# Kernel tuning notes

Measured on AMD Instinct MI355X. Metric: run time of the kernel, lower is better.

## Reference

```python
import jax, jax.numpy as jnp
import numpy as np
from jax import lax

THD = 0.8  # Lowe ratio-test threshold (module init kwarg `thd`)


def setup_inputs() -> dict:
    key = jax.random.key(0)
    k1, k2 = jax.random.split(key)
    desc1 = jax.random.normal(k1, (16384, 128), dtype=jnp.float32)
    desc2 = jax.random.normal(k2, (16384, 128), dtype=jnp.float32)
    return {"desc1": desc1, "desc2": desc2}


def _cdist(a, b):
    # Euclidean pairwise distances, (B1, B2), same math as torch.cdist(p=2)
    sq_a = jnp.sum(a * a, axis=-1, keepdims=True)          # (B1, 1)
    sq_b = jnp.sum(b * b, axis=-1)                          # (B2,)
    d2 = sq_a + sq_b - 2.0 * (a @ b.T)                      # (B1, B2)
    return jnp.sqrt(jnp.maximum(d2, 0.0))


def reference(desc1, desc2):
    cost = _cdist(desc1, desc2)                             # (B1, B2)
    # two smallest distances per row
    neg_vals, idxs_in_2 = lax.top_k(-cost, 2)               # (B1, 2) each
    vals = -neg_vals
    ratio = vals[:, 0] / vals[:, 1]                         # (B1,)
    mask = ratio <= THD                                     # (B1,) bool
    # jit-compatible padded outputs: masked-out rows carry 0 distance; the
    # boolean mask selects the valid (idxs_in1, idxs_in2) match rows, which is
    # the compaction torch does with boolean indexing.
    match_dists = jnp.where(mask, ratio, 0.0)               # (B1,)
    idxs_in1 = jnp.arange(desc1.shape[0], dtype=jnp.int32)
    matches_idxs = jnp.stack([idxs_in1, idxs_in_2[:, 0].astype(jnp.int32)], axis=1)  # (B1, 2)
    return match_dists, matches_idxs, mask
```

## Files before the change

kernel.cpp:

```cpp
#include <hip/hip_runtime.h>
#include <math.h>
#include <float.h>
#include <stdint.h>


typedef __attribute__((ext_vector_type(4))) float     f32x4;
typedef __attribute__((ext_vector_type(8))) _Float16  half8;

#define D_     128
#define BM_    256
#define BN_    32
#define CS_    8
#define PARTS_ 8

__device__ __forceinline__ void gload_lds16(const void* g, void* l) {
  auto gp = (const __attribute__((address_space(1))) unsigned int*)(uintptr_t)g;
  auto lp = (__attribute__((address_space(3))) unsigned int*)(uintptr_t)l;
  __builtin_amdgcn_global_load_lds(gp, lp, 16, 0, 0);
}

__global__ void norms_kernel(const float* __restrict__ d1,
                             const float* __restrict__ d2,
                             float* __restrict__ sq, int B) {
  int gid  = blockIdx.x * blockDim.x + threadIdx.x;
  int wid  = gid >> 6;
  int lane = gid & 63;
  if (wid >= 2 * B) return;
  const float* src = (wid < B) ? (d1 + (size_t)wid * D_)
                               : (d2 + (size_t)(wid - B) * D_);
  float2 v = ((const float2*)src)[lane];
  float s = fmaf(v.x, v.x, v.y * v.y);
  #pragma unroll
  for (int off = 32; off > 0; off >>= 1) s += __shfl_down(s, off, 64);
  if (lane == 0) sq[wid] = s;
}

__global__ void convert_kernel(const float* __restrict__ d1, const float* __restrict__ d2,
                               _Float16* __restrict__ Ahi, _Float16* __restrict__ Alo,
                               _Float16* __restrict__ BhiP, _Float16* __restrict__ BloP,
                               int B) {
  int i = blockIdx.x * blockDim.x + threadIdx.x;
  int total = B * 16;
  if (i >= 2 * total) return;
  bool isB = i >= total;
  int j    = isB ? i - total : i;
  int desc = j >> 4;
  int seg  = j & 15;
  const float* src = (isB ? d2 : d1) + (size_t)desc * D_ + seg * 8;
  float4 v0 = *(const float4*)(src);
  float4 v1 = *(const float4*)(src + 4);
  half8 hv, lv;
  float e[8] = {v0.x, v0.y, v0.z, v0.w, v1.x, v1.y, v1.z, v1.w};
  #pragma unroll
  for (int q = 0; q < 8; ++q) {
    _Float16 h = (_Float16)e[q];
    _Float16 l = (_Float16)(e[q] - (float)h);
    if (isB) { h = (_Float16)(-2.0f) * h; l = (_Float16)(-2.0f) * l; }
    hv[q] = h; lv[q] = l;
  }
  if (!isB) {
    *(half8*)(Ahi + (size_t)desc * D_ + seg * 8) = hv;
    *(half8*)(Alo + (size_t)desc * D_ + seg * 8) = lv;
  } else {
    int t   = desc >> 5, cloc = desc & 31;
    int nf  = cloc >> 4, c15  = cloc & 15;
    int kk  = seg >> 2,  gq   = seg & 3;
    size_t off = (size_t)t * 4096 + kk * 1024 + nf * 512 + gq * 128 + c15 * 8;
    *(half8*)(BhiP + off) = hv;
    *(half8*)(BloP + off) = lv;
  }
}

__global__ __launch_bounds__(256, 2)
void nn_mfma(const _Float16* __restrict__ Ahi, const _Float16* __restrict__ Alo,
             const _Float16* __restrict__ BhiP, const _Float16* __restrict__ BloP,
             const float* __restrict__ sqb,
             float* __restrict__ p_d0, float* __restrict__ p_d1,
             int* __restrict__ p_j0, int B) {
  extern __shared__ char smem[];
  const int tid  = threadIdx.x;
  const int lane = tid & 63;
  const int wid  = tid >> 6;
  const int l15  = lane & 15;
  const int g    = lane >> 4;

  const int nrb   = B / BM_;
  const int rb    = blockIdx.x % nrb;
  const int cspl  = blockIdx.x / nrb;
  const int i0    = rb * BM_;
  const int niter = (B / CS_) / BN_;
  const int tile0 = cspl * niter;

  half8 ah[4][4], al[4][4];
  #pragma unroll
  for (int mf = 0; mf < 4; ++mf) {
    int row = i0 + wid * 64 + mf * 16 + l15;
    const _Float16* pa = Ahi + (size_t)row * D_ + g * 8;
    const _Float16* pl = Alo + (size_t)row * D_ + g * 8;
    #pragma unroll
    for (int kk = 0; kk < 4; ++kk) {
      ah[mf][kk] = *(const half8*)(pa + kk * 32);
      al[mf][kk] = *(const half8*)(pl + kk * 32);
    }
  }

  const _Float16* srcW = ((wid < 2) ? BhiP : BloP)
                       + (size_t)tile0 * 4096 + (wid & 1) * 2048 + lane * 8;
  char* ldsW = smem + (wid >> 1) * 8192 + (wid & 1) * 4096;
  auto stage = [&](int bufbase, int it) {
    const _Float16* s = srcW + (size_t)it * 4096;
    char* l = ldsW + bufbase;
    #pragma unroll
    for (int e = 0; e < 4; ++e) gload_lds16(s + e * 512, l + e * 1024);
  };

  float best0[16], best1[16]; int bj[16];
  #pragma unroll
  for (int s = 0; s < 16; ++s) { best0[s] = FLT_MAX; best1[s] = FLT_MAX; bj[s] = 0x7fffffff; }

  float sjA[2], sjB[2];
  const int colg0 = tile0 * BN_ + l15;

  stage(0, 0);
  #pragma unroll
  for (int nf = 0; nf < 2; ++nf) sjA[nf] = sqb[colg0 + nf * 16];
  __syncthreads();

  auto body = [&](int it, int bufbase, float (&sjc)[2], float (&sjn)[2]) {
    if (it + 1 < niter) {
      stage(bufbase ^ 16384, it + 1);
      #pragma unroll
      for (int nf = 0; nf < 2; ++nf) sjn[nf] = sqb[colg0 + (it + 1) * BN_ + nf * 16];
    }

    f32x4 acc[4][2];
    __builtin_amdgcn_s_setprio(1);
    #pragma unroll
    for (int kk = 0; kk < 4; ++kk) {
      half8 bh[2], bl[2];
      #pragma unroll
      for (int nf = 0; nf < 2; ++nf) {
        bh[nf] = *(const half8*)(smem + bufbase + kk * 2048 + nf * 1024 + lane * 16);
        bl[nf] = *(const half8*)(smem + bufbase + 8192 + kk * 2048 + nf * 1024 + lane * 16);
      }
      #pragma unroll
      for (int mf = 0; mf < 4; ++mf)
        #pragma unroll
        for (int nf = 0; nf < 2; ++nf) {
          if (kk == 0) {
            f32x4 c0 = {sjc[nf], sjc[nf], sjc[nf], sjc[nf]};
            acc[mf][nf] = __builtin_amdgcn_mfma_f32_16x16x32_f16(ah[mf][0], bh[nf], c0, 0, 0, 0);
          } else {
            acc[mf][nf] = __builtin_amdgcn_mfma_f32_16x16x32_f16(ah[mf][kk], bh[nf], acc[mf][nf], 0, 0, 0);
          }
        }
      #pragma unroll
      for (int mf = 0; mf < 4; ++mf)
        #pragma unroll
        for (int nf = 0; nf < 2; ++nf)
          acc[mf][nf] = __builtin_amdgcn_mfma_f32_16x16x32_f16(ah[mf][kk], bl[nf], acc[mf][nf], 0, 0, 0);
      #pragma unroll
      for (int mf = 0; mf < 4; ++mf)
        #pragma unroll
        for (int nf = 0; nf < 2; ++nf)
          acc[mf][nf] = __builtin_amdgcn_mfma_f32_16x16x32_f16(al[mf][kk], bh[nf], acc[mf][nf], 0, 0, 0);
    }
    __builtin_amdgcn_s_setprio(0);

    #pragma unroll
    for (int nf = 0; nf < 2; ++nf) {
      int colg = colg0 + it * BN_ + nf * 16;
      #pragma unroll
      for (int mf = 0; mf < 4; ++mf)
        #pragma unroll
        for (int r = 0; r < 4; ++r) {
          int s = mf * 4 + r;
          float t = acc[mf][nf][r];
          best1[s] = __builtin_amdgcn_fmed3f(t, best0[s], best1[s]);
          bool lt0 = t < best0[s];
          best0[s] = fminf(t, best0[s]);
          bj[s]    = lt0 ? colg : bj[s];
        }
    }
    __syncthreads();
  };

  for (int itp = 0; itp < niter; itp += 2) {
    body(itp,     0,     sjA, sjB);
    body(itp + 1, 16384, sjB, sjA);
  }

  #pragma unroll
  for (int off = 1; off < 16; off <<= 1) {
    #pragma unroll
    for (int s = 0; s < 16; ++s) {
      float e0 = __shfl_xor(best0[s], off, 64);
      float e1 = __shfl_xor(best1[s], off, 64);
      int   f0 = __shfl_xor(bj[s],    off, 64);
      if (e0 < best0[s] || (e0 == best0[s] && f0 < bj[s])) {
        best1[s] = fminf(best0[s], e1);
        best0[s] = e0;
        bj[s]    = f0;
      } else {
        best1[s] = fminf(best1[s], e0);
      }
    }
  }

  if (l15 == 0) {
    #pragma unroll
    for (int s = 0; s < 16; ++s) {
      int mf = s >> 2, r = s & 3;
      int row = i0 + wid * 64 + mf * 16 + g * 4 + r;
      p_d0[row * PARTS_ + cspl] = best0[s];
      p_d1[row * PARTS_ + cspl] = best1[s];
      p_j0[row * PARTS_ + cspl] = bj[s];
    }
  }
}

__global__ void nn_final(const float* __restrict__ sqa,
                         const float* __restrict__ p_d0,
                         const float* __restrict__ p_d1,
                         const int* __restrict__ p_j0,
                         float* __restrict__ out, int B) {
  int row = blockIdx.x * blockDim.x + threadIdx.x;
  if (row >= B) return;
  float d0 = FLT_MAX, d1 = FLT_MAX;
  int j0 = 0x7fffffff;
  for (int cs = 0; cs < PARTS_; ++cs) {
    float e0 = p_d0[row * PARTS_ + cs];
    float e1 = p_d1[row * PARTS_ + cs];
    int   f0 = p_j0[row * PARTS_ + cs];
    if (e0 < d0 || (e0 == d0 && f0 < j0)) {
      d1 = fminf(d0, e1);
      d0 = e0;
      j0 = f0;
    } else {
      d1 = fminf(d1, e0);
    }
  }
  float sa = sqa[row];
  float v0 = sqrtf(fmaxf(sa + d0, 0.f));
  float v1 = sqrtf(fmaxf(sa + d1, 0.f));
  float ratio = v0 / v1;
  bool m = (ratio <= 0.8f);
  out[row]             = m ? ratio : 0.f;
  out[B + row * 2]     = (float)row;
  out[B + row * 2 + 1] = (float)j0;
  out[3 * B + row]     = m ? 1.f : 0.f;
}

extern "C" void kernel_launch(void* const* d_in, const int* in_sizes, int n_in,
                              void* d_out, int out_size, void* d_ws, size_t ws_size,
                              hipStream_t stream) {
  const float* d1 = (const float*)d_in[0];
  const float* d2 = (const float*)d_in[1];
  const int B = in_sizes[0] / D_;

  float* ws   = (float*)d_ws;
  float* sqa  = ws;
  float* sqb  = ws + B;
  float* p_d0 = ws + 2 * B;
  float* p_d1 = ws + 10 * B;
  int*   p_j0 = (int*)(ws + 18 * B);
  _Float16* Ahi  = (_Float16*)(ws + 26 * B);
  _Float16* Alo  = Ahi + (size_t)B * D_;
  _Float16* BhiP = Alo + (size_t)B * D_;
  _Float16* BloP = BhiP + (size_t)B * D_;

  int nthreads = 2 * B * 64;
  norms_kernel<<<(nthreads + 255) / 256, 256, 0, stream>>>(d1, d2, sqa, B);

  int ngroups = 2 * B * 16;
  convert_kernel<<<(ngroups + 255) / 256, 256, 0, stream>>>(d1, d2, Ahi, Alo, BhiP, BloP, B);

  hipFuncSetAttribute((const void*)nn_mfma,
                      hipFuncAttributeMaxDynamicSharedMemorySize, 32768);
  nn_mfma<<<(B / BM_) * CS_, 256, 32768, stream>>>(Ahi, Alo, BhiP, BloP, sqb,
                                                   p_d0, p_d1, p_j0, B);

  nn_final<<<(B + 255) / 256, 256, 0, stream>>>(sqa, p_d0, p_d1, p_j0, (float*)d_out, B);
}
```

Before: 176.1 us.

## Load B tiles directly into registers with single-wave blocks instead of LDS staging

The matching kernel moves from 256-thread blocks that share B tiles through double-buffered LDS to 64-thread single-wave blocks. Each wave loads its B hi/lo fragments straight from global memory into registers, double-buffered across iterations. This removes the LDS traffic and the per-iteration __syncthreads barrier. In exchange there is four times more global/L2 traffic for B, since it is no longer shared across waves, and register pressure rises from holding two B fragment buffers.

```diff
diff --git a/kernel.cpp b/kernel.cpp
--- a/kernel.cpp
+++ b/kernel.cpp
@@ -8,16 +8,10 @@
 typedef __attribute__((ext_vector_type(8))) _Float16  half8;
 
 #define D_     128
-#define BM_    256
+#define WROWS_ 64
 #define BN_    32
 #define CS_    8
 #define PARTS_ 8
-
-__device__ __forceinline__ void gload_lds16(const void* g, void* l) {
-  auto gp = (const __attribute__((address_space(1))) unsigned int*)(uintptr_t)g;
-  auto lp = (__attribute__((address_space(3))) unsigned int*)(uintptr_t)l;
-  __builtin_amdgcn_global_load_lds(gp, lp, 16, 0, 0);
-}
 
 __global__ void norms_kernel(const float* __restrict__ d1,
                              const float* __restrict__ d2,
@@ -71,30 +65,27 @@
   }
 }
 
-__global__ __launch_bounds__(256, 2)
+__global__ __launch_bounds__(64, 2)
 void nn_mfma(const _Float16* __restrict__ Ahi, const _Float16* __restrict__ Alo,
              const _Float16* __restrict__ BhiP, const _Float16* __restrict__ BloP,
              const float* __restrict__ sqb,
              float* __restrict__ p_d0, float* __restrict__ p_d1,
              int* __restrict__ p_j0, int B) {
-  extern __shared__ char smem[];
-  const int tid  = threadIdx.x;
-  const int lane = tid & 63;
-  const int wid  = tid >> 6;
+  const int lane = threadIdx.x & 63;
   const int l15  = lane & 15;
   const int g    = lane >> 4;
 
-  const int nrb   = B / BM_;
+  const int nrb   = B / WROWS_;
   const int rb    = blockIdx.x % nrb;
   const int cspl  = blockIdx.x / nrb;
-  const int i0    = rb * BM_;
+  const int i0    = rb * WROWS_;
   const int niter = (B / CS_) / BN_;
   const int tile0 = cspl * niter;
 
   half8 ah[4][4], al[4][4];
   #pragma unroll
   for (int mf = 0; mf < 4; ++mf) {
-    int row = i0 + wid * 64 + mf * 16 + l15;
+    int row = i0 + mf * 16 + l15;
     const _Float16* pa = Ahi + (size_t)row * D_ + g * 8;
     const _Float16* pl = Alo + (size_t)row * D_ + g * 8;
     #pragma unroll
@@ -104,14 +95,18 @@
     }
   }
 
-  const _Float16* srcW = ((wid < 2) ? BhiP : BloP)
-                       + (size_t)tile0 * 4096 + (wid & 1) * 2048 + lane * 8;
-  char* ldsW = smem + (wid >> 1) * 8192 + (wid & 1) * 4096;
-  auto stage = [&](int bufbase, int it) {
-    const _Float16* s = srcW + (size_t)it * 4096;
-    char* l = ldsW + bufbase;
-    #pragma unroll
-    for (int e = 0; e < 4; ++e) gload_lds16(s + e * 512, l + e * 1024);
+  const _Float16* bH0 = BhiP + (size_t)tile0 * 4096 + lane * 8;
+  const _Float16* bL0 = BloP + (size_t)tile0 * 4096 + lane * 8;
+  auto loadB = [&](half8 (&bh)[4][2], half8 (&bl)[4][2], int it) {
+    const _Float16* pH = bH0 + (size_t)it * 4096;
+    const _Float16* pL = bL0 + (size_t)it * 4096;
+    #pragma unroll
+    for (int kk = 0; kk < 4; ++kk)
+      #pragma unroll
+      for (int nf = 0; nf < 2; ++nf) {
+        bh[kk][nf] = *(const half8*)(pH + kk * 1024 + nf * 512);
+        bl[kk][nf] = *(const half8*)(pL + kk * 1024 + nf * 512);
+      }
   };
 
   float best0[16], best1[16]; int bj[16];
@@ -121,14 +116,17 @@
   float sjA[2], sjB[2];
   const int colg0 = tile0 * BN_ + l15;
 
-  stage(0, 0);
+  half8 bhA[4][2], blA[4][2], bhB[4][2], blB[4][2];
+
+  loadB(bhA, blA, 0);
   #pragma unroll
   for (int nf = 0; nf < 2; ++nf) sjA[nf] = sqb[colg0 + nf * 16];
-  __syncthreads();
-
-  auto body = [&](int it, int bufbase, float (&sjc)[2], float (&sjn)[2]) {
+
+  auto body = [&](int it, half8 (&bhC)[4][2], half8 (&blC)[4][2],
+                  half8 (&bhP)[4][2], half8 (&blP)[4][2],
+                  float (&sjc)[2], float (&sjn)[2]) {
     if (it + 1 < niter) {
-      stage(bufbase ^ 16384, it + 1);
+      loadB(bhP, blP, it + 1);
       #pragma unroll
       for (int nf = 0; nf < 2; ++nf) sjn[nf] = sqb[colg0 + (it + 1) * BN_ + nf * 16];
     }
@@ -137,33 +135,27 @@
     __builtin_amdgcn_s_setprio(1);
     #pragma unroll
     for (int kk = 0; kk < 4; ++kk) {
-      half8 bh[2], bl[2];
-      #pragma unroll
-      for (int nf = 0; nf < 2; ++nf) {
-        bh[nf] = *(const half8*)(smem + bufbase + kk * 2048 + nf * 1024 + lane * 16);
-        bl[nf] = *(const half8*)(smem + bufbase + 8192 + kk * 2048 + nf * 1024 + lane * 16);
-      }
       #pragma unroll
       for (int mf = 0; mf < 4; ++mf)
         #pragma unroll
         for (int nf = 0; nf < 2; ++nf) {
           if (kk == 0) {
             f32x4 c0 = {sjc[nf], sjc[nf], sjc[nf], sjc[nf]};
-            acc[mf][nf] = __builtin_amdgcn_mfma_f32_16x16x32_f16(ah[mf][0], bh[nf], c0, 0, 0, 0);
+            acc[mf][nf] = __builtin_amdgcn_mfma_f32_16x16x32_f16(ah[mf][0], bhC[0][nf], c0, 0, 0, 0);
           } else {
-            acc[mf][nf] = __builtin_amdgcn_mfma_f32_16x16x32_f16(ah[mf][kk], bh[nf], acc[mf][nf], 0, 0, 0);
+            acc[mf][nf] = __builtin_amdgcn_mfma_f32_16x16x32_f16(ah[mf][kk], bhC[kk][nf], acc[mf][nf], 0, 0, 0);
           }
         }
       #pragma unroll
       for (int mf = 0; mf < 4; ++mf)
         #pragma unroll
         for (int nf = 0; nf < 2; ++nf)
-          acc[mf][nf] = __builtin_amdgcn_mfma_f32_16x16x32_f16(ah[mf][kk], bl[nf], acc[mf][nf], 0, 0, 0);
+          acc[mf][nf] = __builtin_amdgcn_mfma_f32_16x16x32_f16(ah[mf][kk], blC[kk][nf], acc[mf][nf], 0, 0, 0);
       #pragma unroll
       for (int mf = 0; mf < 4; ++mf)
         #pragma unroll
         for (int nf = 0; nf < 2; ++nf)
-          acc[mf][nf] = __builtin_amdgcn_mfma_f32_16x16x32_f16(al[mf][kk], bh[nf], acc[mf][nf], 0, 0, 0);
+          acc[mf][nf] = __builtin_amdgcn_mfma_f32_16x16x32_f16(al[mf][kk], bhC[kk][nf], acc[mf][nf], 0, 0, 0);
     }
     __builtin_amdgcn_s_setprio(0);
 
@@ -182,12 +174,11 @@
           bj[s]    = lt0 ? colg : bj[s];
         }
     }
-    __syncthreads();
   };
 
   for (int itp = 0; itp < niter; itp += 2) {
-    body(itp,     0,     sjA, sjB);
-    body(itp + 1, 16384, sjB, sjA);
+    body(itp,     bhA, blA, bhB, blB, sjA, sjB);
+    body(itp + 1, bhB, blB, bhA, blA, sjB, sjA);
   }
 
   #pragma unroll
@@ -211,7 +202,7 @@
     #pragma unroll
     for (int s = 0; s < 16; ++s) {
       int mf = s >> 2, r = s & 3;
-      int row = i0 + wid * 64 + mf * 16 + g * 4 + r;
+      int row = i0 + mf * 16 + g * 4 + r;
       p_d0[row * PARTS_ + cspl] = best0[s];
       p_d1[row * PARTS_ + cspl] = best1[s];
       p_j0[row * PARTS_ + cspl] = bj[s];
@@ -275,10 +266,8 @@
   int ngroups = 2 * B * 16;
   convert_kernel<<<(ngroups + 255) / 256, 256, 0, stream>>>(d1, d2, Ahi, Alo, BhiP, BloP, B);
 
-  hipFuncSetAttribute((const void*)nn_mfma,
-                      hipFuncAttributeMaxDynamicSharedMemorySize, 32768);
-  nn_mfma<<<(B / BM_) * CS_, 256, 32768, stream>>>(Ahi, Alo, BhiP, BloP, sqb,
-                                                   p_d0, p_d1, p_j0, B);
+  nn_mfma<<<(B / WROWS_) * CS_, 64, 0, stream>>>(Ahi, Alo, BhiP, BloP, sqb,
+                                                 p_d0, p_d1, p_j0, B);
 
   nn_final<<<(B + 255) / 256, 256, 0, stream>>>(sqa, p_d0, p_d1, p_j0, (float*)d_out, B);
 }
```

New measurement: 668.4 us. 3.8x slower.

## Software-pipeline top-2 fold with MFMA by splitting N fragments across iterations

Applied to the files above, without the earlier changes.

The inner tile is split into two 16-column halves with separate accumulators. The top-2 fold of the previous iteration's second half is interleaved between the MFMA chains so VALU work can overlap the matrix pipeline. This also cuts live accumulator registers from 8 to 4+4 with a carried state. The cost is one extra fold after the loop, plus a dummy first fold on FLT_MAX values that relies on those never winning.

```diff
diff --git a/kernel.cpp b/kernel.cpp
--- a/kernel.cpp
+++ b/kernel.cpp
@@ -118,8 +118,27 @@
   #pragma unroll
   for (int s = 0; s < 16; ++s) { best0[s] = FLT_MAX; best1[s] = FLT_MAX; bj[s] = 0x7fffffff; }
 
+  auto fold4 = [&](f32x4 (&a)[4], int colg) {
+    #pragma unroll
+    for (int mf = 0; mf < 4; ++mf)
+      #pragma unroll
+      for (int r = 0; r < 4; ++r) {
+        int s = mf * 4 + r;
+        float t = a[mf][r];
+        best1[s] = __builtin_amdgcn_fmed3f(t, best0[s], best1[s]);
+        bool lt0 = t < best0[s];
+        best0[s] = fminf(t, best0[s]);
+        bj[s]    = lt0 ? colg : bj[s];
+      }
+  };
+
   float sjA[2], sjB[2];
   const int colg0 = tile0 * BN_ + l15;
+
+  f32x4 acc1[4];
+  #pragma unroll
+  for (int mf = 0; mf < 4; ++mf)
+    acc1[mf] = (f32x4){FLT_MAX, FLT_MAX, FLT_MAX, FLT_MAX};
 
   stage(0, 0);
   #pragma unroll
@@ -133,55 +152,55 @@
       for (int nf = 0; nf < 2; ++nf) sjn[nf] = sqb[colg0 + (it + 1) * BN_ + nf * 16];
     }
 
-    f32x4 acc[4][2];
+    f32x4 acc0[4];
     __builtin_amdgcn_s_setprio(1);
     #pragma unroll
     for (int kk = 0; kk < 4; ++kk) {
-      half8 bh[2], bl[2];
-      #pragma unroll
-      for (int nf = 0; nf < 2; ++nf) {
-        bh[nf] = *(const half8*)(smem + bufbase + kk * 2048 + nf * 1024 + lane * 16);
-        bl[nf] = *(const half8*)(smem + bufbase + 8192 + kk * 2048 + nf * 1024 + lane * 16);
+      half8 bh = *(const half8*)(smem + bufbase + kk * 2048 + lane * 16);
+      half8 bl = *(const half8*)(smem + bufbase + 8192 + kk * 2048 + lane * 16);
+      #pragma unroll
+      for (int mf = 0; mf < 4; ++mf) {
+        if (kk == 0) {
+          f32x4 c0 = {sjc[0], sjc[0], sjc[0], sjc[0]};
+          acc0[mf] = __builtin_amdgcn_mfma_f32_16x16x32_f16(ah[mf][0], bh, c0, 0, 0, 0);
+        } else {
+          acc0[mf] = __builtin_amdgcn_mfma_f32_16x16x32_f16(ah[mf][kk], bh, acc0[mf], 0, 0, 0);
+        }
       }
       #pragma unroll
       for (int mf = 0; mf < 4; ++mf)
-        #pragma unroll
-        for (int nf = 0; nf < 2; ++nf) {
-          if (kk == 0) {
-            f32x4 c0 = {sjc[nf], sjc[nf], sjc[nf], sjc[nf]};
-            acc[mf][nf] = __builtin_amdgcn_mfma_f32_16x16x32_f16(ah[mf][0], bh[nf], c0, 0, 0, 0);
-          } else {
-            acc[mf][nf] = __builtin_amdgcn_mfma_f32_16x16x32_f16(ah[mf][kk], bh[nf], acc[mf][nf], 0, 0, 0);
-          }
+        acc0[mf] = __builtin_amdgcn_mfma_f32_16x16x32_f16(ah[mf][kk], bl, acc0[mf], 0, 0, 0);
+      #pragma unroll
+      for (int mf = 0; mf < 4; ++mf)
+        acc0[mf] = __builtin_amdgcn_mfma_f32_16x16x32_f16(al[mf][kk], bh, acc0[mf], 0, 0, 0);
+    }
+
+    fold4(acc1, colg0 + (it - 1) * BN_ + 16);
+
+    #pragma unroll
+    for (int kk = 0; kk < 4; ++kk) {
+      half8 bh = *(const half8*)(smem + bufbase + kk * 2048 + 1024 + lane * 16);
+      half8 bl = *(const half8*)(smem + bufbase + 8192 + kk * 2048 + 1024 + lane * 16);
+      #pragma unroll
+      for (int mf = 0; mf < 4; ++mf) {
+        if (kk == 0) {
+          f32x4 c1 = {sjc[1], sjc[1], sjc[1], sjc[1]};
+          acc1[mf] = __builtin_amdgcn_mfma_f32_16x16x32_f16(ah[mf][0], bh, c1, 0, 0, 0);
+        } else {
+          acc1[mf] = __builtin_amdgcn_mfma_f32_16x16x32_f16(ah[mf][kk], bh, acc1[mf], 0, 0, 0);
         }
+      }
       #pragma unroll
       for (int mf = 0; mf < 4; ++mf)
-        #pragma unroll
-        for (int nf = 0; nf < 2; ++nf)
-          acc[mf][nf] = __builtin_amdgcn_mfma_f32_16x16x32_f16(ah[mf][kk], bl[nf], acc[mf][nf], 0, 0, 0);
+        acc1[mf] = __builtin_amdgcn_mfma_f32_16x16x32_f16(ah[mf][kk], bl, acc1[mf], 0, 0, 0);
       #pragma unroll
       for (int mf = 0; mf < 4; ++mf)
-        #pragma unroll
-        for (int nf = 0; nf < 2; ++nf)
-          acc[mf][nf] = __builtin_amdgcn_mfma_f32_16x16x32_f16(al[mf][kk], bh[nf], acc[mf][nf], 0, 0, 0);
+        acc1[mf] = __builtin_amdgcn_mfma_f32_16x16x32_f16(al[mf][kk], bh, acc1[mf], 0, 0, 0);
     }
     __builtin_amdgcn_s_setprio(0);
 
-    #pragma unroll
-    for (int nf = 0; nf < 2; ++nf) {
-      int colg = colg0 + it * BN_ + nf * 16;
-      #pragma unroll
-      for (int mf = 0; mf < 4; ++mf)
-        #pragma unroll
-        for (int r = 0; r < 4; ++r) {
-          int s = mf * 4 + r;
-          float t = acc[mf][nf][r];
-          best1[s] = __builtin_amdgcn_fmed3f(t, best0[s], best1[s]);
-          bool lt0 = t < best0[s];
-          best0[s] = fminf(t, best0[s]);
-          bj[s]    = lt0 ? colg : bj[s];
-        }
-    }
+    fold4(acc0, colg0 + it * BN_);
+
     __syncthreads();
   };
 
@@ -189,6 +208,7 @@
     body(itp,     0,     sjA, sjB);
     body(itp + 1, 16384, sjB, sjA);
   }
+  fold4(acc1, colg0 + (niter - 1) * BN_ + 16);
 
   #pragma unroll
   for (int off = 1; off < 16; off <<= 1) {
```

After: 373.0 us. 2.12x slower.

## Triple-buffer B tiles with fine-grained vmcnt waits and preload column norms to LDS

Applied to the files above, without the earlier changes.

Replaces the double-buffered B-tile pipeline with a three-buffer ring that prefetches two tiles ahead. Each iteration now waits with explicit vmcnt counts and a raw s_barrier instead of __syncthreads, so the global-to-LDS load can overlap more MFMA work. The block's column norms are preloaded once into LDS, replacing per-iteration global loads. LDS per block grows from 32 KB to 56 KB, which could limit occupancy, and the hand-written waitcnt logic is fragile.

```diff
diff --git a/kernel.cpp b/kernel.cpp
--- a/kernel.cpp
+++ b/kernel.cpp
@@ -78,6 +78,7 @@
              float* __restrict__ p_d0, float* __restrict__ p_d1,
              int* __restrict__ p_j0, int B) {
   extern __shared__ char smem[];
+  float* sq_lds = (float*)(smem + 49152);
   const int tid  = threadIdx.x;
   const int lane = tid & 63;
   const int wid  = tid >> 6;
@@ -104,6 +105,16 @@
     }
   }
 
+  {
+    const float* sqs = sqb + cspl * 2048;
+    #pragma unroll
+    for (int e = 0; e < 2; ++e) {
+      int idx = tid + e * 256;
+      float4 v = ((const float4*)sqs)[idx];
+      ((float4*)sq_lds)[idx] = v;
+    }
+  }
+
   const _Float16* srcW = ((wid < 2) ? BhiP : BloP)
                        + (size_t)tile0 * 4096 + (wid & 1) * 2048 + lane * 8;
   char* ldsW = smem + (wid >> 1) * 8192 + (wid & 1) * 4096;
@@ -118,19 +129,25 @@
   #pragma unroll
   for (int s = 0; s < 16; ++s) { best0[s] = FLT_MAX; best1[s] = FLT_MAX; bj[s] = 0x7fffffff; }
 
-  float sjA[2], sjB[2];
   const int colg0 = tile0 * BN_ + l15;
 
   stage(0, 0);
-  #pragma unroll
-  for (int nf = 0; nf < 2; ++nf) sjA[nf] = sqb[colg0 + nf * 16];
-  __syncthreads();
-
-  auto body = [&](int it, int bufbase, float (&sjc)[2], float (&sjn)[2]) {
+  stage(16384, 1);
+  asm volatile("s_waitcnt vmcnt(4)" ::: "memory");
+  asm volatile("s_waitcnt lgkmcnt(0)" ::: "memory");
+  __builtin_amdgcn_s_barrier();
+  asm volatile("" ::: "memory");
+
+  float sjc0 = sq_lds[l15];
+  float sjc1 = sq_lds[16 + l15];
+
+  int bcur = 0, bstage = 32768;
+  for (int it = 0; it < niter; ++it) {
+    if (it + 2 < niter) stage(bstage, it + 2);
+    float sjn0 = 0.f, sjn1 = 0.f;
     if (it + 1 < niter) {
-      stage(bufbase ^ 16384, it + 1);
-      #pragma unroll
-      for (int nf = 0; nf < 2; ++nf) sjn[nf] = sqb[colg0 + (it + 1) * BN_ + nf * 16];
+      sjn0 = sq_lds[(it + 1) * 32 + l15];
+      sjn1 = sq_lds[(it + 1) * 32 + 16 + l15];
     }
 
     f32x4 acc[4][2];
@@ -140,15 +157,16 @@
       half8 bh[2], bl[2];
       #pragma unroll
       for (int nf = 0; nf < 2; ++nf) {
-        bh[nf] = *(const half8*)(smem + bufbase + kk * 2048 + nf * 1024 + lane * 16);
-        bl[nf] = *(const half8*)(smem + bufbase + 8192 + kk * 2048 + nf * 1024 + lane * 16);
+        bh[nf] = *(const half8*)(smem + bcur + kk * 2048 + nf * 1024 + lane * 16);
+        bl[nf] = *(const half8*)(smem + bcur + 8192 + kk * 2048 + nf * 1024 + lane * 16);
       }
       #pragma unroll
       for (int mf = 0; mf < 4; ++mf)
         #pragma unroll
         for (int nf = 0; nf < 2; ++nf) {
           if (kk == 0) {
-            f32x4 c0 = {sjc[nf], sjc[nf], sjc[nf], sjc[nf]};
+            float sj = nf ? sjc1 : sjc0;
+            f32x4 c0 = {sj, sj, sj, sj};
             acc[mf][nf] = __builtin_amdgcn_mfma_f32_16x16x32_f16(ah[mf][0], bh[nf], c0, 0, 0, 0);
           } else {
             acc[mf][nf] = __builtin_amdgcn_mfma_f32_16x16x32_f16(ah[mf][kk], bh[nf], acc[mf][nf], 0, 0, 0);
@@ -182,12 +200,15 @@
           bj[s]    = lt0 ? colg : bj[s];
         }
     }
-    __syncthreads();
-  };
-
-  for (int itp = 0; itp < niter; itp += 2) {
-    body(itp,     0,     sjA, sjB);
-    body(itp + 1, 16384, sjB, sjA);
+
+    if (it + 2 < niter) asm volatile("s_waitcnt vmcnt(4)" ::: "memory");
+    else                asm volatile("s_waitcnt vmcnt(0)" ::: "memory");
+    __builtin_amdgcn_s_barrier();
+    asm volatile("" ::: "memory");
+
+    sjc0 = sjn0; sjc1 = sjn1;
+    bcur   = (bcur   == 32768) ? 0 : bcur   + 16384;
+    bstage = (bstage == 32768) ? 0 : bstage + 16384;
   }
 
   #pragma unroll
@@ -276,8 +297,8 @@
   convert_kernel<<<(ngroups + 255) / 256, 256, 0, stream>>>(d1, d2, Ahi, Alo, BhiP, BloP, B);
 
   hipFuncSetAttribute((const void*)nn_mfma,
-                      hipFuncAttributeMaxDynamicSharedMemorySize, 32768);
-  nn_mfma<<<(B / BM_) * CS_, 256, 32768, stream>>>(Ahi, Alo, BhiP, BloP, sqb,
+                      hipFuncAttributeMaxDynamicSharedMemorySize, 57344);
+  nn_mfma<<<(B / BM_) * CS_, 256, 57344, stream>>>(Ahi, Alo, BhiP, BloP, sqb,
                                                    p_d0, p_d1, p_j0, B);
 
   nn_final<<<(B + 255) / 256, 256, 0, stream>>>(sqa, p_d0, p_d1, p_j0, (float*)d_out, B);
```

Result: no change. 175.4 us (-0.4%).
